# Performance work log

Measured on AMD Instinct MI355X. Metric: run time of the kernel, lower is better.

The kernel has to match this reference:

```python
import jax, jax.numpy as jnp
import numpy as np

T = 48  # top-T from init

def setup_inputs() -> dict:
    key = jax.random.key(0)
    ks = jax.random.split(key, 8)
    B, C, H, W = 16, 512, 32, 32
    tc = C // 8
    return {
        "x": jax.random.normal(ks[0], (B, C, H, W), jnp.float32),
        "fW": jax.random.normal(ks[1], (tc, C), jnp.float32) * 0.05,
        "fb": jax.random.normal(ks[2], (tc,), jnp.float32) * 0.05,
        "gW": jax.random.normal(ks[3], (tc, C), jnp.float32) * 0.05,
        "gb": jax.random.normal(ks[4], (tc,), jnp.float32) * 0.05,
        "hW": jax.random.normal(ks[5], (C, C), jnp.float32) * 0.05,
        "hb": jax.random.normal(ks[6], (C,), jnp.float32) * 0.05,
        "scale": jax.random.normal(ks[7], (1,), jnp.float32),
    }

def reference(x, fW, fb, gW, gb, hW, hb, scale):
    B, C, H, W = x.shape
    tc = fW.shape[0]
    HW = H * W
    # normalize by Frobenius norm over (batch, channel) -> [H, W]
    xn = x / jnp.linalg.norm(x, axis=(0, 1))[None, None]  # [B,C,H,W]
    # 1x1 convs, output already channel-last [B,H,W,out]
    f = jnp.einsum('bchw,oc->bhwo', xn, fW) + fb          # [B,H,W,tc]
    g = jnp.einsum('bchw,oc->bhwo', xn, gW) + gb          # [B,H,W,tc]
    h = jnp.einsum('bchw,oc->bhwo', xn, hW) + hb          # [B,H,W,C]
    xp = jnp.transpose(xn, (0, 2, 3, 1))                  # [B,H,W,C]
    # scores: queries H-major, keys W-major (faithful to permute(0,3,2,1).reshape)
    g_keys = jnp.transpose(g, (0, 3, 2, 1)).reshape(B, tc, HW)  # [B,tc,W*H]
    s = jnp.matmul(f.reshape(B, HW, tc), g_keys)          # [B,HW,HW]
    beta = jax.nn.softmax(s, axis=-1)
    o = jnp.matmul(beta, h.reshape(B, HW, C)).reshape(B, H, W, C)
    fdd = scale * o + xp                                  # [B,H,W,C]
    # per-batch correlation: fdd[b] ([H,W,C]) @ fdd[b].reshape(C,HW)
    corr = jnp.einsum('bhwc,bcn->bhwn', fdd, fdd.reshape(B, C, HW))  # [B,H,W,HW]
    top = jax.lax.top_k(corr, T)[0]                       # descending top-T values
    top = jax.nn.relu(top)
    top = top / jnp.linalg.norm(top, axis=(0, 1))[None, None]  # norm over (B,H) -> [W,T]
    return jnp.transpose(top, (0, 3, 1, 2))               # [B,T,H,W]
```

## Files before the change

### kernel.cpp

```cpp
#include <hip/hip_runtime.h>
#include <cstdint>
#include <cstddef>

#define B_   16
#define C_   512
#define H_   32
#define W_   32
#define HW_  1024
#define TC_  64
#define T_   48

typedef unsigned short u16;
typedef __attribute__((ext_vector_type(8))) short short8v;
typedef __attribute__((ext_vector_type(4))) float f32x4;

__device__ __forceinline__ u16 tobf(float x) {
    unsigned u = __float_as_uint(x);
    return (u16)((u + 0x7FFFu + ((u >> 16) & 1u)) >> 16);
}
__device__ __forceinline__ float frombf(u16 h) {
    return __uint_as_float(((unsigned)h) << 16);
}

__device__ __forceinline__ void gld16(const void* g, void* l) {
    __builtin_amdgcn_global_load_lds(
        (const __attribute__((address_space(1))) void*)g,
        (__attribute__((address_space(3))) void*)l, 16, 0, 0);
}

__global__ void k_colsq(const float* __restrict__ x, float* __restrict__ partial) {
    int bid = blockIdx.x;
    int col = (bid & 3) * 256 + threadIdx.x;
    int r0  = (bid >> 2) * 256;
    const float* p = x + (size_t)r0 * HW_ + col;
    float s = 0.f;
    for (int r = 0; r < 256; ++r) { float v = p[(size_t)r * HW_]; s += v * v; }
    partial[(size_t)(bid >> 2) * HW_ + col] = s;
}

__global__ void k_rsqrt(const float* __restrict__ partial, float* __restrict__ ninv) {
    int i = blockIdx.x * 256 + threadIdx.x;
    if (i < HW_) {
        float s = 0.f;
        for (int r = 0; r < 32; ++r) s += partial[(size_t)r * HW_ + i];
        ninv[i] = rsqrtf(s);
    }
}

__global__ void k_transpose(const float* __restrict__ x, const float* __restrict__ ninv,
                            u16* __restrict__ obH) {
    __shared__ float tile[32][33];
    int b  = blockIdx.z;
    int m0 = blockIdx.x * 32, c0 = blockIdx.y * 32;
    int tx = threadIdx.x, ty = threadIdx.y;
    const float* xb = x + (size_t)b * C_ * HW_;
    #pragma unroll
    for (int j = 0; j < 32; j += 8)
        tile[ty + j][tx] = xb[(size_t)(c0 + ty + j) * HW_ + m0 + tx];
    __syncthreads();
    size_t base = (size_t)b * HW_ * C_;
    #pragma unroll
    for (int j = 0; j < 32; j += 8) {
        int m = m0 + ty + j;
        obH[base + (size_t)m * C_ + c0 + tx] = tobf(tile[tx][ty + j] * ninv[m]);
    }
}

__global__ void k_packW(const float* __restrict__ in, u16* __restrict__ oh) {
    size_t i = (size_t)blockIdx.x * 256 + threadIdx.x;
    oh[i] = tobf(in[i]);
}
__global__ void k_packFG(const float* __restrict__ fW, const float* __restrict__ gW,
                         const float* __restrict__ fb, const float* __restrict__ gb,
                         u16* __restrict__ oh, float* __restrict__ fgb) {
    int idx = blockIdx.x * 256 + threadIdx.x;
    int row = idx >> 9, c = idx & 511;
    float v = (row < 64) ? fW[row * 512 + c] : gW[(row - 64) * 512 + c];
    oh[idx] = tobf(v);
    if (idx < 128) fgb[idx] = (idx < 64) ? fb[idx] : gb[idx - 64];
}

template<int PERMB, int EPI, int KU>
__global__ __launch_bounds__(256) void k_gemm1(
    const u16* __restrict__ A, const u16* __restrict__ Bm,
    const float* __restrict__ bias,
    float* __restrict__ Cf, u16* __restrict__ Ch,
    const float* __restrict__ scaleP,
    int N, int K, int lda, int ldb, long sA, long sB, long sC)
{
    __shared__ u16 lds[8192 * KU];
    const int b = blockIdx.z;
    const u16* pA = A + (size_t)b * sA;
    const u16* pB = Bm + (size_t)b * sB;
    const int m0 = blockIdx.y * 128, n0 = blockIdx.x * 128;
    const int tid = threadIdx.x, wave = tid >> 6, lane = tid & 63;
    const int wm = wave >> 1, wn = wave & 1;
    const int g = lane >> 4;

    f32x4 acc[4][4];
    #pragma unroll
    for (int i = 0; i < 4; ++i)
        #pragma unroll
        for (int j = 0; j < 4; ++j) { f32x4 z = {0.f,0.f,0.f,0.f}; acc[i][j] = z; }

    for (int kt = 0; kt < (K >> 5); kt += KU) {
        __syncthreads();
        #pragma unroll
        for (int u = 0; u < KU; ++u) {
            const int k0 = (kt + u) << 5;
            u16* lb = lds + u * 8192;
            #pragma unroll
            for (int q = 0; q < 4; ++q) {
                int ci = wave * 4 + q;
                bool isA = ci < 8;
                int li = ci & 7;
                const u16* gp = isA ? pA : pB;
                int ld = isA ? lda : ldb;
                int rb = isA ? m0 : n0;
                int rp = li * 8 + (lane >> 3);
                int gg = (lane & 7) ^ (rp & 7);
                int r  = rp * 2 + (gg >> 2);
                int kc = k0 + (gg & 3) * 8;
                int rowg = rb + r;
                if (PERMB && !isA) rowg = ((rowg & 31) << 5) | (rowg >> 5);
                gld16(gp + (size_t)rowg * ld + kc,
                      lb + (isA ? 0 : 4096) + li * 512 + lane * 8);
            }
        }
        __syncthreads();
        #pragma unroll
        for (int u = 0; u < KU; ++u) {
            const u16* As = lds + u * 8192;
            const u16* Bs = As + 4096;
            short8v av[4];
            #pragma unroll
            for (int i = 0; i < 4; ++i) {
                int r = wm * 64 + i * 16 + (lane & 15);
                int rp = r >> 1, gg = ((r & 1) << 2) + g;
                av[i] = *(const short8v*)(As + rp * 64 + ((gg ^ (rp & 7)) << 3));
            }
            #pragma unroll
            for (int j = 0; j < 4; ++j) {
                int r = wn * 64 + j * 16 + (lane & 15);
                int rp = r >> 1, gg = ((r & 1) << 2) + g;
                short8v bv = *(const short8v*)(Bs + rp * 64 + ((gg ^ (rp & 7)) << 3));
                #pragma unroll
                for (int i = 0; i < 4; ++i)
                    acc[i][j] = __builtin_amdgcn_mfma_f32_16x16x32_bf16(av[i], bv, acc[i][j], 0, 0, 0);
            }
        }
    }

    const float sc = (EPI == 2) ? scaleP[0] : 0.f;
    const int colbase = n0 + wn * 64 + (lane & 15);
    const int rowbase = m0 + wm * 64 + ((lane >> 4) << 2);
    #pragma unroll
    for (int i = 0; i < 4; ++i)
        #pragma unroll
        for (int j = 0; j < 4; ++j) {
            int col = colbase + j * 16;
            #pragma unroll
            for (int rg = 0; rg < 4; ++rg) {
                int row = rowbase + i * 16 + rg;
                size_t idx = (size_t)b * sC + (size_t)row * N + col;
                float a = acc[i][j][rg];
                if (EPI == 0)      Cf[idx] = a;
                else if (EPI == 2) Ch[idx] = tobf(sc * a + frombf(Ch[idx]));
                else if (EPI == 4) Ch[idx] = tobf(a);
                else if (EPI == 5) Ch[idx] = tobf(a + bias[row]);
                else               Ch[idx] = tobf(a + bias[col]);
            }
        }
}

template<int PERMB, int EPI, int KU>
__global__ __launch_bounds__(512) void k_gemm2(
    const u16* __restrict__ A, const u16* __restrict__ Bm,
    const float* __restrict__ bias,
    float* __restrict__ Cf, u16* __restrict__ Ch,
    const float* __restrict__ scaleP,
    int N, int K, int lda, int ldb, long sA, long sB, long sC)
{
    __shared__ u16 lds[12288 * KU];
    const int b = blockIdx.z;
    const u16* pA = A + (size_t)b * sA;
    const u16* pB = Bm + (size_t)b * sB;
    const int m0 = blockIdx.y * 128, n0 = blockIdx.x * 256;
    const int tid = threadIdx.x, wave = tid >> 6, lane = tid & 63;
    const int wm = wave >> 2, wn = wave & 3;
    const int g = lane >> 4;

    f32x4 acc[4][4];
    #pragma unroll
    for (int i = 0; i < 4; ++i)
        #pragma unroll
        for (int j = 0; j < 4; ++j) { f32x4 z = {0.f,0.f,0.f,0.f}; acc[i][j] = z; }

    for (int kt = 0; kt < (K >> 5); kt += KU) {
        __syncthreads();
        #pragma unroll
        for (int u = 0; u < KU; ++u) {
            const int k0 = (kt + u) << 5;
            u16* lb = lds + u * 12288;
            #pragma unroll
            for (int q = 0; q < 3; ++q) {
                int ci = wave * 3 + q;
                bool isA = ci < 8;
                int li = isA ? ci : ci - 8;
                const u16* gp = isA ? pA : pB;
                int ld = isA ? lda : ldb;
                int rb = isA ? m0 : n0;
                int rp = li * 8 + (lane >> 3);
                int gg = (lane & 7) ^ (rp & 7);
                int r  = rp * 2 + (gg >> 2);
                int kc = k0 + (gg & 3) * 8;
                int rowg = rb + r;
                if (PERMB && !isA) rowg = ((rowg & 31) << 5) | (rowg >> 5);
                gld16(gp + (size_t)rowg * ld + kc,
                      lb + (isA ? 0 : 4096) + li * 512 + lane * 8);
            }
        }
        __syncthreads();
        #pragma unroll
        for (int u = 0; u < KU; ++u) {
            const u16* As = lds + u * 12288;
            const u16* Bs = As + 4096;
            short8v av[4];
            #pragma unroll
            for (int i = 0; i < 4; ++i) {
                int r = wm * 64 + i * 16 + (lane & 15);
                int rp = r >> 1, gg = ((r & 1) << 2) + g;
                av[i] = *(const short8v*)(As + rp * 64 + ((gg ^ (rp & 7)) << 3));
            }
            #pragma unroll
            for (int j = 0; j < 4; ++j) {
                int r = wn * 64 + j * 16 + (lane & 15);
                int rp = r >> 1, gg = ((r & 1) << 2) + g;
                short8v bv = *(const short8v*)(Bs + rp * 64 + ((gg ^ (rp & 7)) << 3));
                #pragma unroll
                for (int i = 0; i < 4; ++i)
                    acc[i][j] = __builtin_amdgcn_mfma_f32_16x16x32_bf16(av[i], bv, acc[i][j], 0, 0, 0);
            }
        }
    }

    const float sc = (EPI == 2) ? scaleP[0] : 0.f;
    const int colbase = n0 + wn * 64 + (lane & 15);
    const int rowbase = m0 + wm * 64 + ((lane >> 4) << 2);
    #pragma unroll
    for (int i = 0; i < 4; ++i)
        #pragma unroll
        for (int j = 0; j < 4; ++j) {
            int col = colbase + j * 16;
            #pragma unroll
            for (int rg = 0; rg < 4; ++rg) {
                int row = rowbase + i * 16 + rg;
                size_t idx = (size_t)b * sC + (size_t)row * N + col;
                float a = acc[i][j][rg];
                if (EPI == 0)      Cf[idx] = a;
                else if (EPI == 2) Ch[idx] = tobf(sc * a + frombf(Ch[idx]));
                else if (EPI == 4) Ch[idx] = tobf(a);
                else if (EPI == 5) Ch[idx] = tobf(a + bias[row]);
                else               Ch[idx] = tobf(a + bias[col]);
            }
        }
}

__global__ __launch_bounds__(256) void k_softmax(u16* __restrict__ S) {
    size_t row = blockIdx.x;
    u16* r = S + row * (size_t)HW_;
    int t = threadIdx.x;
    ushort4 raw = ((const ushort4*)r)[t];
    float v0 = frombf(raw.x), v1 = frombf(raw.y), v2 = frombf(raw.z), v3 = frombf(raw.w);

    __shared__ float redm[4], reds[4];
    int wid = t >> 6, lane = t & 63;

    float m = fmaxf(fmaxf(v0, v1), fmaxf(v2, v3));
    for (int o = 32; o > 0; o >>= 1) m = fmaxf(m, __shfl_down(m, o));
    if (lane == 0) redm[wid] = m;
    __syncthreads();
    if (t == 0) redm[0] = fmaxf(fmaxf(redm[0], redm[1]), fmaxf(redm[2], redm[3]));
    __syncthreads();
    m = redm[0];

    v0 = expf(v0 - m); v1 = expf(v1 - m); v2 = expf(v2 - m); v3 = expf(v3 - m);
    float s = v0 + v1 + v2 + v3;
    for (int o = 32; o > 0; o >>= 1) s += __shfl_down(s, o);
    if (lane == 0) reds[wid] = s;
    __syncthreads();
    if (t == 0) reds[0] = reds[0] + reds[1] + reds[2] + reds[3];
    __syncthreads();
    float inv = 1.f / reds[0];
    ushort4 o4;
    o4.x = tobf(v0 * inv); o4.y = tobf(v1 * inv);
    o4.z = tobf(v2 * inv); o4.w = tobf(v3 * inv);
    ((ushort4*)r)[t] = o4;
}

__global__ void k_tposeU1(const u16* __restrict__ src, u16* __restrict__ dst) {
    __shared__ u16 tile[32][33];
    int b = blockIdx.z;
    const u16* sb = src + (size_t)b * (C_ * HW_);
    u16* db = dst + (size_t)b * (C_ * HW_);
    int c0 = blockIdx.x * 32, r0 = blockIdx.y * 32;
    int tx = threadIdx.x, ty = threadIdx.y;
    #pragma unroll
    for (int j = 0; j < 32; j += 8)
        tile[ty + j][tx] = sb[(size_t)(r0 + ty + j) * HW_ + c0 + tx];
    __syncthreads();
    #pragma unroll
    for (int j = 0; j < 32; j += 8)
        db[(size_t)(c0 + ty + j) * C_ + r0 + tx] = tile[tx][ty + j];
}

__device__ __forceinline__ float sort64_desc(float v, int lane) {
    #pragma unroll
    for (int k = 2; k <= 64; k <<= 1) {
        #pragma unroll
        for (int j = k >> 1; j > 0; j >>= 1) {
            float o = __shfl_xor(v, j);
            bool takeMax = (((lane & k) == 0) == ((lane & j) == 0));
            v = takeMax ? fmaxf(v, o) : fminf(v, o);
        }
    }
    return v;
}
__device__ __forceinline__ float bmerge64_desc(float a, float b, int lane) {
    float br = __shfl(b, 63 - lane);
    float c = fmaxf(a, br);
    #pragma unroll
    for (int j = 32; j > 0; j >>= 1) {
        float o = __shfl_xor(c, j);
        c = ((lane & j) == 0) ? fmaxf(c, o) : fminf(c, o);
    }
    return c;
}

__global__ __launch_bounds__(256) void k_topk(const float* __restrict__ corr,
                                              float* __restrict__ topv) {
    int row = blockIdx.x, tid = threadIdx.x, wave = tid >> 6, lane = tid & 63;
    const float4 e = ((const float4*)(corr + (size_t)row * HW_))[tid];
    float gm = fmaxf(fmaxf(e.x, e.y), fmaxf(e.z, e.w));
    float v = sort64_desc(gm, lane);

    __shared__ float ls[4][64];
    __shared__ float tau_s;
    __shared__ int cnt_s;
    __shared__ float buf[1024];
    ls[wave][lane] = v;
    buf[tid] = -INFINITY; buf[tid + 256] = -INFINITY;
    buf[tid + 512] = -INFINITY; buf[tid + 768] = -INFINITY;
    if (tid == 0) cnt_s = 0;
    __syncthreads();

    if (wave == 0) {
        float ab = bmerge64_desc(ls[0][lane], ls[1][lane], lane);
        float cd = bmerge64_desc(ls[2][lane], ls[3][lane], lane);
        float t  = bmerge64_desc(ab, cd, lane);
        if (lane == T_ - 1) tau_s = t;
    }
    __syncthreads();
    float tau = tau_s;

    int c = (e.x >= tau) + (e.y >= tau) + (e.z >= tau) + (e.w >= tau);
    int off = 0;
    if (c) off = atomicAdd(&cnt_s, c);
    if (e.x >= tau) buf[off++] = e.x;
    if (e.y >= tau) buf[off++] = e.y;
    if (e.z >= tau) buf[off++] = e.z;
    if (e.w >= tau) buf[off++] = e.w;
    __syncthreads();
    int cnt = cnt_s;

    if (cnt <= 128) {
        if (wave == 0) {
            float a  = sort64_desc(buf[lane], lane);
            float b2 = sort64_desc(buf[64 + lane], lane);
            float br = __shfl(b2, 63 - lane);
            float hi = fmaxf(a, br);
            #pragma unroll
            for (int j = 32; j > 0; j >>= 1) {
                float o = __shfl_xor(hi, j);
                hi = ((lane & j) == 0) ? fmaxf(hi, o) : fminf(hi, o);
            }
            if (lane < T_) topv[(size_t)row * T_ + lane] = fmaxf(hi, 0.f);
        }
    } else {
        int P = 256; while (P < cnt) P <<= 1;
        for (int k = 2; k <= P; k <<= 1)
            for (int j = k >> 1; j > 0; j >>= 1) {
                for (int t2 = tid; t2 < P; t2 += 256) {
                    int ixj = t2 ^ j;
                    if (ixj > t2) {
                        float a = buf[t2], b3 = buf[ixj];
                        bool desc = ((t2 & k) == 0);
                        if (desc ? (a < b3) : (a > b3)) { buf[t2] = b3; buf[ixj] = a; }
                    }
                }
                __syncthreads();
            }
        if (tid < T_) topv[(size_t)row * T_ + tid] = fmaxf(buf[tid], 0.f);
    }
}

__global__ void k_colss(const float* __restrict__ topv, float* __restrict__ colss) {
    int o = blockIdx.x;
    int w = o / T_, t = o % T_;
    int lane = threadIdx.x;
    float s = 0.f;
    for (int i = lane; i < 512; i += 64) {
        int b = i >> 5, h = i & 31;
        float v = topv[(size_t)((b << 10) + (h << 5) + w) * T_ + t];
        s += v * v;
    }
    for (int off = 32; off > 0; off >>= 1) s += __shfl_down(s, off);
    if (lane == 0) colss[o] = s;
}

__global__ void k_final(const float* __restrict__ topv, const float* __restrict__ colss,
                        float* __restrict__ out) {
    int idx = blockIdx.x * 256 + threadIdx.x;
    if (idx >= B_ * T_ * HW_) return;
    int w = idx & 31;
    int h = (idx >> 5) & 31;
    int t = (idx >> 10) % T_;
    int b = idx / (T_ * HW_);
    float v = topv[(size_t)((b << 10) + (h << 5) + w) * T_ + t];
    out[idx] = v * rsqrtf(colss[w * T_ + t]);
}

extern "C" void kernel_launch(void* const* d_in, const int* in_sizes, int n_in,
                              void* d_out, int out_size, void* d_ws, size_t ws_size,
                              hipStream_t stream) {
    const float* x     = (const float*)d_in[0];
    const float* fW    = (const float*)d_in[1];
    const float* fb    = (const float*)d_in[2];
    const float* gW    = (const float*)d_in[3];
    const float* gb    = (const float*)d_in[4];
    const float* hW    = (const float*)d_in[5];
    const float* hb    = (const float*)d_in[6];
    const float* scale = (const float*)d_in[7];
    float* out = (float*)d_out;

    char* wsb = (char*)d_ws;
    float* part = (float*)(wsb + 0);
    float* ninv = (float*)(wsb + 131072);
    u16*   hWh  = (u16*)(wsb + 135168);
    u16*   fgWh = (u16*)(wsb + 1183744);
    float* fgb  = (float*)(wsb + 1445888);
    u16*   xnH  = (u16*)(wsb + 1446400);
    u16*   fgH  = (u16*)(wsb + 35000832);
    u16*   fgL  = (u16*)(wsb + 39195136);
    u16*   hvTH = (u16*)(wsb + 43389440);
    float* S    = (float*)(wsb + 76943872);
    float* topv = (float*)fgH;
    float* colss= (float*)fgL;
    u16*   Sp   = (u16*)S;

    const long sXn = 524288;
    const long sFG = 131072;
    const long sS  = 1048576;

    k_colsq<<<128, 256, 0, stream>>>(x, part);
    k_rsqrt<<<4, 256, 0, stream>>>(part, ninv);

    k_transpose<<<dim3(32, 16, 16), dim3(32, 8), 0, stream>>>(x, ninv, xnH);

    k_packW<<<1024, 256, 0, stream>>>(hW, hWh);
    k_packFG<<<256, 256, 0, stream>>>(fW, gW, fb, gb, fgWh, fgb);

    k_gemm1<0, 6, 2><<<dim3(1, 8, 16), 256, 0, stream>>>(
        xnH, fgWh, fgb, nullptr, fgH, nullptr,
        128, 512, 512, 512, sXn, 0, sFG);

    k_gemm2<0, 5, 2><<<dim3(4, 4, 16), 512, 0, stream>>>(
        hWh, xnH, hb, nullptr, hvTH, nullptr,
        1024, 512, 512, 512, 0, sXn, sXn);

    k_gemm2<1, 4, 2><<<dim3(4, 8, 16), 512, 0, stream>>>(
        fgH, fgH + 64, nullptr, nullptr, Sp, nullptr,
        1024, 64, 128, 128, sFG, sFG, sS);

    k_softmax<<<B_ * HW_, 256, 0, stream>>>(Sp);

    k_gemm1<0, 2, 2><<<dim3(4, 8, 16), 256, 0, stream>>>(
        Sp, hvTH, nullptr, nullptr, xnH, scale,
        512, 1024, 1024, 1024, sS, sXn, sXn);

    k_tposeU1<<<dim3(32, 16, 16), dim3(32, 8), 0, stream>>>(xnH, hvTH);

    k_gemm2<0, 0, 2><<<dim3(4, 8, 16), 512, 0, stream>>>(
        xnH, hvTH, nullptr, S, nullptr, nullptr,
        1024, 512, 512, 512, sXn, sXn, sS);

    k_topk<<<B_ * HW_, 256, 0, stream>>>(S, topv);

    k_colss<<<W_ * T_, 64, 0, stream>>>(topv, colss);
    k_final<<<(B_ * T_ * HW_ + 255) / 256, 256, 0, stream>>>(topv, colss, out);
}
```

Measured before the change: 218.2 us.

## Process one top-k row per wavefront and switch beta@h GEMM to larger tile kernel

The top-k kernel now assigns one row per 64-lane wavefront (four rows per block) instead of one row per 256-thread block. This replaces shared-memory atomics and block barriers with a wave-level prefix scan and shuffles. The threshold now comes from a single wave sort of per-lane maxima over 16 elements. Separately, the attention-output GEMM uses the 512-thread gemm2 variant with half as many blocks along x. The wave-local top-k avoids sync overhead, but the fallback bitonic sort now runs on only 64 lanes, which is slower whenever more than 128 candidates pass the threshold.

```diff
diff --git a/kernel.cpp b/kernel.cpp
--- a/kernel.cpp
+++ b/kernel.cpp
@@ -339,68 +339,68 @@
 
 __global__ __launch_bounds__(256) void k_topk(const float* __restrict__ corr,
                                               float* __restrict__ topv) {
-    int row = blockIdx.x, tid = threadIdx.x, wave = tid >> 6, lane = tid & 63;
-    const float4 e = ((const float4*)(corr + (size_t)row * HW_))[tid];
-    float gm = fmaxf(fmaxf(e.x, e.y), fmaxf(e.z, e.w));
-    float v = sort64_desc(gm, lane);
-
-    __shared__ float ls[4][64];
-    __shared__ float tau_s;
-    __shared__ int cnt_s;
-    __shared__ float buf[1024];
-    ls[wave][lane] = v;
-    buf[tid] = -INFINITY; buf[tid + 256] = -INFINITY;
-    buf[tid + 512] = -INFINITY; buf[tid + 768] = -INFINITY;
-    if (tid == 0) cnt_s = 0;
-    __syncthreads();
-
-    if (wave == 0) {
-        float ab = bmerge64_desc(ls[0][lane], ls[1][lane], lane);
-        float cd = bmerge64_desc(ls[2][lane], ls[3][lane], lane);
-        float t  = bmerge64_desc(ab, cd, lane);
-        if (lane == T_ - 1) tau_s = t;
-    }
-    __syncthreads();
-    float tau = tau_s;
-
-    int c = (e.x >= tau) + (e.y >= tau) + (e.z >= tau) + (e.w >= tau);
-    int off = 0;
-    if (c) off = atomicAdd(&cnt_s, c);
-    if (e.x >= tau) buf[off++] = e.x;
-    if (e.y >= tau) buf[off++] = e.y;
-    if (e.z >= tau) buf[off++] = e.z;
-    if (e.w >= tau) buf[off++] = e.w;
-    __syncthreads();
-    int cnt = cnt_s;
-
-    if (cnt <= 128) {
-        if (wave == 0) {
-            float a  = sort64_desc(buf[lane], lane);
-            float b2 = sort64_desc(buf[64 + lane], lane);
-            float br = __shfl(b2, 63 - lane);
-            float hi = fmaxf(a, br);
-            #pragma unroll
-            for (int j = 32; j > 0; j >>= 1) {
-                float o = __shfl_xor(hi, j);
-                hi = ((lane & j) == 0) ? fmaxf(hi, o) : fminf(hi, o);
-            }
-            if (lane < T_) topv[(size_t)row * T_ + lane] = fmaxf(hi, 0.f);
-        }
+    __shared__ float buf[4][1024];
+    int wave = threadIdx.x >> 6, lane = threadIdx.x & 63;
+    int row = blockIdx.x * 4 + wave;
+    const float4* rp = (const float4*)(corr + (size_t)row * HW_);
+
+    float4 e[4];
+    #pragma unroll
+    for (int q = 0; q < 4; ++q) e[q] = rp[lane * 4 + q];
+
+    float gm = -INFINITY;
+    #pragma unroll
+    for (int q = 0; q < 4; ++q)
+        gm = fmaxf(gm, fmaxf(fmaxf(e[q].x, e[q].y), fmaxf(e[q].z, e[q].w)));
+    float sorted = sort64_desc(gm, lane);
+    float tau = __shfl(sorted, T_ - 1);
+
+    int c = 0;
+    #pragma unroll
+    for (int q = 0; q < 4; ++q)
+        c += (e[q].x >= tau) + (e[q].y >= tau) + (e[q].z >= tau) + (e[q].w >= tau);
+    int sc = c;
+    #pragma unroll
+    for (int o = 1; o < 64; o <<= 1) {
+        int t2 = __shfl_up(sc, o);
+        if (lane >= o) sc += t2;
+    }
+    int off = sc - c;
+    int cnt = __shfl(sc, 63);
+
+    float* wb = buf[wave];
+    #pragma unroll
+    for (int q = 0; q < 4; ++q) {
+        if (e[q].x >= tau) wb[off++] = e[q].x;
+        if (e[q].y >= tau) wb[off++] = e[q].y;
+        if (e[q].z >= tau) wb[off++] = e[q].z;
+        if (e[q].w >= tau) wb[off++] = e[q].w;
+    }
+
+    float* orow = topv + (size_t)row * T_;
+    if (cnt <= 64) {
+        float a = (lane < cnt) ? wb[lane] : -INFINITY;
+        a = sort64_desc(a, lane);
+        if (lane < T_) orow[lane] = fmaxf(a, 0.f);
+    } else if (cnt <= 128) {
+        float a  = sort64_desc(wb[lane], lane);
+        float b2 = sort64_desc((lane < cnt - 64) ? wb[64 + lane] : -INFINITY, lane);
+        float m2 = bmerge64_desc(a, b2, lane);
+        if (lane < T_) orow[lane] = fmaxf(m2, 0.f);
     } else {
         int P = 256; while (P < cnt) P <<= 1;
+        for (int i = cnt + lane; i < P; i += 64) wb[i] = -INFINITY;
         for (int k = 2; k <= P; k <<= 1)
-            for (int j = k >> 1; j > 0; j >>= 1) {
-                for (int t2 = tid; t2 < P; t2 += 256) {
+            for (int j = k >> 1; j > 0; j >>= 1)
+                for (int t2 = lane; t2 < P; t2 += 64) {
                     int ixj = t2 ^ j;
                     if (ixj > t2) {
-                        float a = buf[t2], b3 = buf[ixj];
+                        float a = wb[t2], b3 = wb[ixj];
                         bool desc = ((t2 & k) == 0);
-                        if (desc ? (a < b3) : (a > b3)) { buf[t2] = b3; buf[ixj] = a; }
+                        if (desc ? (a < b3) : (a > b3)) { wb[t2] = b3; wb[ixj] = a; }
                     }
                 }
-                __syncthreads();
-            }
-        if (tid < T_) topv[(size_t)row * T_ + tid] = fmaxf(buf[tid], 0.f);
+        if (lane < T_) orow[lane] = fmaxf(wb[lane], 0.f);
     }
 }
 
@@ -484,7 +484,7 @@
 
     k_softmax<<<B_ * HW_, 256, 0, stream>>>(Sp);
 
-    k_gemm1<0, 2, 2><<<dim3(4, 8, 16), 256, 0, stream>>>(
+    k_gemm2<0, 2, 2><<<dim3(2, 8, 16), 512, 0, stream>>>(
         Sp, hvTH, nullptr, nullptr, xnH, scale,
         512, 1024, 1024, 1024, sS, sXn, sXn);
 
@@ -494,7 +494,7 @@
         xnH, hvTH, nullptr, S, nullptr, nullptr,
         1024, 512, 512, 512, sXn, sXn, sS);
 
-    k_topk<<<B_ * HW_, 256, 0, stream>>>(S, topv);
+    k_topk<<<B_ * HW_ / 4, 256, 0, stream>>>(S, topv);
 
     k_colss<<<W_ * T_, 64, 0, stream>>>(topv, colss);
     k_final<<<(B_ * T_ * HW_ + 255) / 256, 256, 0, stream>>>(topv, colss, out);
```

After: 220.4 us. Within noise of the previous version (+1.0%).
